# Performance work log

Measured on AMD Instinct MI355X. Metric: run time of the kernel, lower is better.

## Reference

```python
import jax, jax.numpy as jnp
import numpy as np

H, A, V = 8, 32, 32
NODE_IN, EDGE_IN, NODE_OUT, EDGE_OUT = 128, 64, 128, 64


def setup_inputs() -> dict:
    key = jax.random.key(0)
    ks = jax.random.split(key, 8)
    B, N = 1, 384
    s = lambda fan: 1.0 / np.sqrt(fan).astype(np.float32)
    nodes = jax.random.normal(ks[0], (B, NODE_IN, N), jnp.float32)
    edges = jax.random.normal(ks[1], (B, EDGE_IN, N, N), jnp.float32)
    mask = jax.random.randint(ks[2], (B, N), 0, 2).astype(bool)
    W_q = jax.random.normal(ks[3], (A * H, NODE_IN), jnp.float32) * s(NODE_IN)
    W_k = jax.random.normal(ks[4], (A * H, NODE_IN + EDGE_IN), jnp.float32) * s(NODE_IN + EDGE_IN)
    W_v = jax.random.normal(ks[5], (V * H, NODE_IN + EDGE_IN), jnp.float32) * s(NODE_IN + EDGE_IN)
    W_o = jax.random.normal(ks[6], (NODE_OUT, V * H), jnp.float32) * s(V * H)
    W_e = jax.random.normal(ks[7], (EDGE_OUT, V * H + EDGE_IN), jnp.float32) * s(V * H + EDGE_IN)
    return dict(nodes=nodes, edges=edges, mask=mask, W_q=W_q, W_k=W_k, W_v=W_v, W_o=W_o, W_e=W_e)


def reference(nodes, edges, mask, W_q, W_k, W_v, W_o, W_e):
    B, C, N = nodes.shape
    # 1x1 convs are channel matmuls
    query = jnp.einsum('oc,bcn->bon', W_q, nodes)                      # [B, H*A, N]
    node_edges = jnp.concatenate(
        [jnp.broadcast_to(nodes[:, :, :, None], (B, C, N, N)), edges], axis=1)  # [B, C+E, N, N]
    key = jnp.einsum('oc,bcij->boij', W_k, node_edges)                 # [B, H*A, N, N]
    value = jnp.einsum('oc,bcij->boij', W_v, node_edges).reshape(B, H, V, N, N)
    # elementwise QK: query broadcast over column axis j
    sim = (query[:, :, :, None] * key).reshape(B, H, A, N, N).sum(axis=2)
    sim = sim / jnp.sqrt(jnp.asarray(A, sim.dtype))                    # [B, H, N, N]
    sim = jnp.where(mask[:, None, None, :], sim, -jnp.inf)
    sim = jax.nn.softmax(sim, axis=-1)
    mm = (mask[:, None, :, None] & mask[:, None, None, :]).astype(sim.dtype)  # [B,1,N,N]
    sim = sim * mm
    value = value * mm[:, None]
    node_features = jnp.einsum('bhij,bhvij->bhvi', sim, value).reshape(B, H * V, N)
    node_out = jnp.einsum('od,bdn->bon', W_o, node_features)           # [B, node_out, N]
    # symmetrized edge features: (f_i + f_j) / 2, then concat raw edges
    ef = (node_features[:, :, :, None] + node_features[:, :, None, :]) * 0.5  # [B,H*V,N,N]
    ef = jnp.concatenate([ef, edges], axis=1)
    edge_out = jnp.einsum('oc,bcij->boij', W_e, ef)                    # [B, edge_out, N, N]
    return node_out, edge_out
```

## Files before the change

### kernel.cpp

```cpp
#include <hip/hip_runtime.h>
#include <math.h>

#define NN 384
#define NSQ (NN*NN)

#define WS_MASKF 0
#define WS_C1    384
#define WS_P     3456
#define WS_VN    200064
#define WS_T     298368
#define WS_GH    494976
#define WS_WT    519552
#define WS_WOT   523648
#define WS_WVE   556416
#define WS_WEN   572800

typedef short short8 __attribute__((ext_vector_type(8)));
typedef float f32x4 __attribute__((ext_vector_type(4)));

__device__ __forceinline__ unsigned short f2bf(float x) {
    unsigned u = __float_as_uint(x);
    return (unsigned short)((u + 0x7FFFu + ((u >> 16) & 1u)) >> 16);
}

__global__ __launch_bounds__(256) void k_proj(
    const float* __restrict__ nodes, const float* __restrict__ Wq,
    const float* __restrict__ Wk, const float* __restrict__ Wv,
    const float* __restrict__ Wo, const float* __restrict__ We,
    const unsigned int* __restrict__ mi, float* __restrict__ ws) {
    int tid = threadIdx.x;
    if (blockIdx.x >= 96) {
        if (blockIdx.x == 96) {
            __shared__ int bytemode;
            if (tid == 0) bytemode = 0;
            __syncthreads();
            unsigned v0 = mi[tid];
            unsigned v1 = (tid < 128) ? mi[256 + tid] : 0u;
            if (v0 > 1u || v1 > 1u) bytemode = 1;
            __syncthreads();
            float* maskf = ws + WS_MASKF;
            for (int j = tid; j < NN; j += 256) {
                int on;
                if (bytemode) on = (((const unsigned char*)mi)[j] != 0);
                else          on = (mi[j] != 0u);
                maskf[j] = on ? 1.0f : 0.0f;
            }
        } else if (blockIdx.x == 97) {
            unsigned short* WtBF = reinterpret_cast<unsigned short*>(ws + WS_WT);
            for (int idx = tid; idx < 4096; idx += 256) {
                int o = idx >> 6, c = idx & 63;
                WtBF[o * 64 + c] = f2bf(We[o * 320 + 256 + c]);
            }
        } else if (blockIdx.x == 98) {
            float* WoT = ws + WS_WOT;
            for (int idx = tid; idx < 32768; idx += 256) {
                int dd = idx >> 7, o = idx & 127;
                WoT[dd * 128 + o] = Wo[o * 256 + dd];
            }
        } else if (blockIdx.x == 99) {
            float* WvE = ws + WS_WVE;
            for (int idx = tid; idx < 16384; idx += 256) {
                int c = idx >> 8, d = idx & 255;
                WvE[c * 256 + d] = Wv[d * 192 + 128 + c];
            }
        } else {
            float* WeN = ws + WS_WEN;
            for (int idx = tid; idx < 16384; idx += 256) {
                int dd = idx >> 6, o = idx & 63;
                WeN[dd * 64 + o] = We[o * 320 + dd];
            }
        }
        return;
    }
    float* c1_ws = ws + WS_C1;
    float* P_ws  = ws + WS_P;
    float* vn_ws = ws + WS_VN;
    int i0 = blockIdx.x * 4;
    __shared__ float nl[128][4];
    __shared__ float q_l[256][4];
    __shared__ float qk_l[256][4];
    for (int idx = tid; idx < 512; idx += 256) {
        int m = idx >> 2, ii = idx & 3;
        nl[m][ii] = nodes[m * NN + i0 + ii];
    }
    __syncthreads();
    int o = tid;
    float aq[4], ak[4], av[4];
#pragma unroll
    for (int ii = 0; ii < 4; ii++) { aq[ii] = 0.f; ak[ii] = 0.f; av[ii] = 0.f; }
    {
        const float4* wq4 = reinterpret_cast<const float4*>(Wq + o * 128);
        const float4* wk4 = reinterpret_cast<const float4*>(Wk + o * 192);
        const float4* wv4 = reinterpret_cast<const float4*>(Wv + o * 192);
#pragma unroll 8
        for (int m4 = 0; m4 < 32; m4++) {
            float4 wq = wq4[m4];
            float4 wk = wk4[m4];
            float4 wv = wv4[m4];
#pragma unroll
            for (int s = 0; s < 4; s++) {
                int m = m4 * 4 + s;
                float fq = s == 0 ? wq.x : s == 1 ? wq.y : s == 2 ? wq.z : wq.w;
                float fk = s == 0 ? wk.x : s == 1 ? wk.y : s == 2 ? wk.z : wk.w;
                float fv = s == 0 ? wv.x : s == 1 ? wv.y : s == 2 ? wv.z : wv.w;
#pragma unroll
                for (int ii = 0; ii < 4; ii++) {
                    float nv = nl[m][ii];
                    aq[ii] = fmaf(fq, nv, aq[ii]);
                    ak[ii] = fmaf(fk, nv, ak[ii]);
                    av[ii] = fmaf(fv, nv, av[ii]);
                }
            }
        }
    }
#pragma unroll
    for (int ii = 0; ii < 4; ii++) {
        vn_ws[(size_t)(i0 + ii) * 256 + o] = av[ii];
        q_l[o][ii]  = aq[ii];
        qk_l[o][ii] = aq[ii] * ak[ii];
    }
    __syncthreads();
    if (tid < 32) {
        int h = tid >> 2, ii = tid & 3;
        float s = 0.f;
        for (int a = 0; a < 32; a++) s += qk_l[h * 32 + a][ii];
        c1_ws[(i0 + ii) * 8 + h] = s;
    }
    for (int rep = 0; rep < 2; rep++) {
        int idx = rep * 256 + tid;
        int c = idx & 63, h = idx >> 6;
        float ap[4];
#pragma unroll
        for (int ii = 0; ii < 4; ii++) ap[ii] = 0.f;
        for (int a = 0; a < 32; a++) {
            float w = Wk[(h * 32 + a) * 192 + 128 + c];
#pragma unroll
            for (int ii = 0; ii < 4; ii++)
                ap[ii] = fmaf(q_l[h * 32 + a][ii], w, ap[ii]);
        }
#pragma unroll
        for (int ii = 0; ii < 4; ii++)
            P_ws[(size_t)(i0 + ii) * 512 + c * 8 + h] = ap[ii];
    }
}

__global__ __launch_bounds__(512) void k_attn(
    const float* __restrict__ edges, const float* __restrict__ ws_ro,
    float* __restrict__ gh_ws, float* __restrict__ out) {
    __shared__ __align__(16) unsigned short epad_h[64 * 392];
    __shared__ __align__(16) float sT2[NN * 8];
    __shared__ __align__(16) float T_lds[512];
    __shared__ float nf_lds[256];
    const float* maskf = ws_ro + WS_MASKF;
    const float* c1w   = ws_ro + WS_C1;
    const float* Pw    = ws_ro + WS_P;
    const float* vn_ws = ws_ro + WS_VN;
    const float* WvE   = ws_ro + WS_WVE;
    const float* WoT   = ws_ro + WS_WOT;
    const float* WeN   = ws_ro + WS_WEN;
    int i = blockIdx.x;
    int tid = threadIdx.x;
    int wv = tid >> 6, ln = tid & 63;
    float mask_i = maskf[i];

    if (tid < NN) {
        int j = tid;
        const float* eb = edges + (size_t)i * NN + j;
        const float* Pi = Pw + (size_t)i * 512;
        float acc[8];
#pragma unroll
        for (int h = 0; h < 8; h++) acc[h] = 0.f;
#pragma unroll
        for (int cb = 0; cb < 4; cb++) {
            float ev[16];
#pragma unroll
            for (int t = 0; t < 16; t++)
                ev[t] = eb[(size_t)(cb * 16 + t) * NSQ];
#pragma unroll
            for (int t = 0; t < 16; t++) {
                int c = cb * 16 + t;
                epad_h[c * 392 + j] = f2bf(ev[t]);
                const float* Pc = Pi + c * 8;
#pragma unroll
                for (int h = 0; h < 8; h++) acc[h] = fmaf(Pc[h], ev[t], acc[h]);
            }
        }
        float mj = maskf[j];
        const float* c1i = c1w + i * 8;
        float sv[8];
#pragma unroll
        for (int h = 0; h < 8; h++) {
            float s = (c1i[h] + acc[h]) * 0.17677669529663687f;
            sv[h] = (mj != 0.0f) ? s : -1e30f;
        }
        *reinterpret_cast<float4*>(&sT2[j * 8])     = make_float4(sv[0], sv[1], sv[2], sv[3]);
        *reinterpret_cast<float4*>(&sT2[j * 8 + 4]) = make_float4(sv[4], sv[5], sv[6], sv[7]);
    }
    __syncthreads();
    float v[6];
    {
        int h = wv;
#pragma unroll
        for (int k = 0; k < 6; k++) v[k] = sT2[(ln + 64 * k) * 8 + h];
    }
    __syncthreads();
    {
        int h = wv;
        float m = v[0];
#pragma unroll
        for (int k = 1; k < 6; k++) m = fmaxf(m, v[k]);
#pragma unroll
        for (int s = 1; s < 64; s <<= 1) m = fmaxf(m, __shfl_xor(m, s));
        float ex[6]; float sum = 0.f;
#pragma unroll
        for (int k = 0; k < 6; k++) { ex[k] = __expf(v[k] - m); sum += ex[k]; }
#pragma unroll
        for (int s = 1; s < 64; s <<= 1) sum += __shfl_xor(sum, s);
        float fac = mask_i / sum;
        unsigned short* s_bf = reinterpret_cast<unsigned short*>(sT2);
#pragma unroll
        for (int k = 0; k < 6; k++)
            s_bf[h * 392 + ln + 64 * k] = f2bf(ex[k] * fac);
    }
    __syncthreads();
    if (tid < 256) {
        const unsigned short* s_bf = reinterpret_cast<const unsigned short*>(sT2);
        int nc   = ln & 15;
        int quad = ln >> 4;
        int hrow = nc & 7;
        f32x4 acc = {0.f, 0.f, 0.f, 0.f};
#pragma unroll
        for (int s = 0; s < 12; s++) {
            int jb = s * 32 + quad * 8;
            short8 a = *reinterpret_cast<const short8*>(&s_bf[hrow * 392 + jb]);
            short8 b = *reinterpret_cast<const short8*>(&epad_h[(wv * 16 + nc) * 392 + jb]);
            acc = __builtin_amdgcn_mfma_f32_16x16x32_bf16(a, b, acc, 0, 0, 0);
        }
        if (ln < 32) {
#pragma unroll
            for (int r = 0; r < 4; r++) {
                int h = quad * 4 + r;
                T_lds[h * 64 + wv * 16 + nc] = acc[r];
            }
        }
    }
    __syncthreads();
    if (tid < 256) {
        int d = tid, h = d >> 5;
        float a0 = 0.f, a1 = 0.f, a2 = 0.f, a3 = 0.f;
#pragma unroll
        for (int c = 0; c < 64; c += 4) {
            a0 = fmaf(WvE[(c    ) * 256 + d], T_lds[h * 64 + c    ], a0);
            a1 = fmaf(WvE[(c + 1) * 256 + d], T_lds[h * 64 + c + 1], a1);
            a2 = fmaf(WvE[(c + 2) * 256 + d], T_lds[h * 64 + c + 2], a2);
            a3 = fmaf(WvE[(c + 3) * 256 + d], T_lds[h * 64 + c + 3], a3);
        }
        nf_lds[d] = mask_i * vn_ws[(size_t)i * 256 + d] + ((a0 + a1) + (a2 + a3));
    }
    __syncthreads();
    if (tid < 128) {
        int o = tid;
        float b0 = 0.f, b1 = 0.f, b2 = 0.f, b3 = 0.f;
#pragma unroll 8
        for (int dd = 0; dd < 256; dd += 4) {
            b0 = fmaf(WoT[(dd    ) * 128 + o], nf_lds[dd    ], b0);
            b1 = fmaf(WoT[(dd + 1) * 128 + o], nf_lds[dd + 1], b1);
            b2 = fmaf(WoT[(dd + 2) * 128 + o], nf_lds[dd + 2], b2);
            b3 = fmaf(WoT[(dd + 3) * 128 + o], nf_lds[dd + 3], b3);
        }
        out[o * NN + i] = (b0 + b1) + (b2 + b3);
    } else if (tid < 192) {
        int o = tid - 128;
        float b0 = 0.f, b1 = 0.f, b2 = 0.f, b3 = 0.f;
#pragma unroll 8
        for (int dd = 0; dd < 256; dd += 4) {
            b0 = fmaf(WeN[(dd    ) * 64 + o], nf_lds[dd    ], b0);
            b1 = fmaf(WeN[(dd + 1) * 64 + o], nf_lds[dd + 1], b1);
            b2 = fmaf(WeN[(dd + 2) * 64 + o], nf_lds[dd + 2], b2);
            b3 = fmaf(WeN[(dd + 3) * 64 + o], nf_lds[dd + 3], b3);
        }
        gh_ws[o * NN + i] = 0.5f * ((b0 + b1) + (b2 + b3));
    }
}

__global__ __launch_bounds__(192) void k_edge(
    const float* __restrict__ edges, const float* __restrict__ ws_ro,
    float* __restrict__ out_e) {
    __shared__ __align__(16) unsigned short eT[48 * 72];
    const unsigned short* WtBF = reinterpret_cast<const unsigned short*>(ws_ro + WS_WT);
    const float* gh = ws_ro + WS_GH;
    int i = blockIdx.x, jh = blockIdx.y, tid = threadIdx.x;

    {
        int ch = tid / 48, jl = tid - ch * 48;
        int c0 = ch * 16;
        const float* eb = edges + (size_t)c0 * NSQ + (size_t)i * NN + jh * 48 + jl;
        float ev[16];
#pragma unroll
        for (int t = 0; t < 16; t++)
            ev[t] = eb[(size_t)t * NSQ];
        short8 p0, p1;
#pragma unroll
        for (int t = 0; t < 8; t++) p0[t] = (short)f2bf(ev[t]);
#pragma unroll
        for (int t = 0; t < 8; t++) p1[t] = (short)f2bf(ev[t + 8]);
        *reinterpret_cast<short8*>(&eT[jl * 72 + c0])     = p0;
        *reinterpret_cast<short8*>(&eT[jl * 72 + c0 + 8]) = p1;
    }
    __syncthreads();

    int L = tid & 63, wv = tid >> 6;
    int nc = L & 15, quad = L >> 4;
    short8 a00 = *reinterpret_cast<const short8*>(&WtBF[(0 * 16 + nc) * 64 + 0  + quad * 8]);
    short8 a01 = *reinterpret_cast<const short8*>(&WtBF[(0 * 16 + nc) * 64 + 32 + quad * 8]);
    short8 a10 = *reinterpret_cast<const short8*>(&WtBF[(1 * 16 + nc) * 64 + 0  + quad * 8]);
    short8 a11 = *reinterpret_cast<const short8*>(&WtBF[(1 * 16 + nc) * 64 + 32 + quad * 8]);
    short8 a20 = *reinterpret_cast<const short8*>(&WtBF[(2 * 16 + nc) * 64 + 0  + quad * 8]);
    short8 a21 = *reinterpret_cast<const short8*>(&WtBF[(2 * 16 + nc) * 64 + 32 + quad * 8]);
    short8 a30 = *reinterpret_cast<const short8*>(&WtBF[(3 * 16 + nc) * 64 + 0  + quad * 8]);
    short8 a31 = *reinterpret_cast<const short8*>(&WtBF[(3 * 16 + nc) * 64 + 32 + quad * 8]);
    float ghi[16];
#pragma unroll
    for (int ot = 0; ot < 4; ot++)
#pragma unroll
        for (int r = 0; r < 4; r++)
            ghi[ot * 4 + r] = gh[(ot * 16 + quad * 4 + r) * NN + i];

    {
        int jt = wv;
        short8 b0 = *reinterpret_cast<const short8*>(&eT[(jt * 16 + nc) * 72 + 0  + quad * 8]);
        short8 b1 = *reinterpret_cast<const short8*>(&eT[(jt * 16 + nc) * 72 + 32 + quad * 8]);
        int j = jh * 48 + jt * 16 + nc;
        f32x4 c0 = {0.f, 0.f, 0.f, 0.f};
        f32x4 c1 = {0.f, 0.f, 0.f, 0.f};
        f32x4 c2 = {0.f, 0.f, 0.f, 0.f};
        f32x4 c3 = {0.f, 0.f, 0.f, 0.f};
        c0 = __builtin_amdgcn_mfma_f32_16x16x32_bf16(a00, b0, c0, 0, 0, 0);
        c0 = __builtin_amdgcn_mfma_f32_16x16x32_bf16(a01, b1, c0, 0, 0, 0);
        c1 = __builtin_amdgcn_mfma_f32_16x16x32_bf16(a10, b0, c1, 0, 0, 0);
        c1 = __builtin_amdgcn_mfma_f32_16x16x32_bf16(a11, b1, c1, 0, 0, 0);
        c2 = __builtin_amdgcn_mfma_f32_16x16x32_bf16(a20, b0, c2, 0, 0, 0);
        c2 = __builtin_amdgcn_mfma_f32_16x16x32_bf16(a21, b1, c2, 0, 0, 0);
        c3 = __builtin_amdgcn_mfma_f32_16x16x32_bf16(a30, b0, c3, 0, 0, 0);
        c3 = __builtin_amdgcn_mfma_f32_16x16x32_bf16(a31, b1, c3, 0, 0, 0);
#pragma unroll
        for (int ot = 0; ot < 4; ot++) {
            f32x4 cc = ot == 0 ? c0 : ot == 1 ? c1 : ot == 2 ? c2 : c3;
#pragma unroll
            for (int r = 0; r < 4; r++) {
                int o = ot * 16 + quad * 4 + r;
                float val = cc[r] + ghi[ot * 4 + r] + gh[o * NN + j];
                __builtin_nontemporal_store(val, &out_e[(size_t)o * NSQ + (size_t)i * NN + j]);
            }
        }
    }
}

extern "C" void kernel_launch(void* const* d_in, const int* in_sizes, int n_in,
                              void* d_out, int out_size, void* d_ws, size_t ws_size,
                              hipStream_t stream) {
    const float* nodes = (const float*)d_in[0];
    const float* edges = (const float*)d_in[1];
    const unsigned int* mask = (const unsigned int*)d_in[2];
    const float* Wq = (const float*)d_in[3];
    const float* Wk = (const float*)d_in[4];
    const float* Wv = (const float*)d_in[5];
    const float* Wo = (const float*)d_in[6];
    const float* We = (const float*)d_in[7];
    float* out = (float*)d_out;
    float* ws  = (float*)d_ws;
    float* out_e = out + 128 * NN;

    hipLaunchKernelGGL(k_proj, dim3(101), dim3(256), 0, stream,
                       nodes, Wq, Wk, Wv, Wo, We, mask, ws);
    hipLaunchKernelGGL(k_attn, dim3(384), dim3(512), 0, stream,
                       edges, ws, ws + WS_GH, out);
    hipLaunchKernelGGL(k_edge, dim3(384, 8), dim3(192), 0, stream,
                       edges, ws, out_e);
}
```

Before: 143.5 us.

## Split attention over column halves with flash-style softmax merge kernel

```diff
diff --git a/kernel.cpp b/kernel.cpp
--- a/kernel.cpp
+++ b/kernel.cpp
@@ -8,12 +8,13 @@
 #define WS_C1    384
 #define WS_P     3456
 #define WS_VN    200064
-#define WS_T     298368
 #define WS_GH    494976
 #define WS_WT    519552
 #define WS_WOT   523648
 #define WS_WVE   556416
 #define WS_WEN   572800
+#define WS_TP    602112
+#define WS_MS    995328
 
 typedef short short8 __attribute__((ext_vector_type(8)));
 typedef float f32x4 __attribute__((ext_vector_type(4)));
@@ -21,6 +22,9 @@
 __device__ __forceinline__ unsigned short f2bf(float x) {
     unsigned u = __float_as_uint(x);
     return (unsigned short)((u + 0x7FFFu + ((u >> 16) & 1u)) >> 16);
+}
+__device__ __forceinline__ float bf2f(unsigned short b) {
+    return __uint_as_float(((unsigned)b) << 16);
 }
 
 __global__ __launch_bounds__(256) void k_proj(
@@ -145,45 +149,54 @@
 }
 
 __global__ __launch_bounds__(512) void k_attn(
-    const float* __restrict__ edges, const float* __restrict__ ws_ro,
-    float* __restrict__ gh_ws, float* __restrict__ out) {
-    __shared__ __align__(16) unsigned short epad_h[64 * 392];
-    __shared__ __align__(16) float sT2[NN * 8];
-    __shared__ __align__(16) float T_lds[512];
-    __shared__ float nf_lds[256];
-    const float* maskf = ws_ro + WS_MASKF;
-    const float* c1w   = ws_ro + WS_C1;
-    const float* Pw    = ws_ro + WS_P;
-    const float* vn_ws = ws_ro + WS_VN;
-    const float* WvE   = ws_ro + WS_WVE;
-    const float* WoT   = ws_ro + WS_WOT;
-    const float* WeN   = ws_ro + WS_WEN;
-    int i = blockIdx.x;
+    const float* __restrict__ edges, float* __restrict__ ws) {
+    __shared__ __align__(16) unsigned short epad_h[64 * 200];
+    __shared__ __align__(16) float sT2[192 * 8];
+    const float* maskf = ws + WS_MASKF;
+    const float* c1w   = ws + WS_C1;
+    const float* Pw    = ws + WS_P;
+    int i = blockIdx.x, jh = blockIdx.y;
     int tid = threadIdx.x;
     int wv = tid >> 6, ln = tid & 63;
-    float mask_i = maskf[i];
-
-    if (tid < NN) {
-        int j = tid;
-        const float* eb = edges + (size_t)i * NN + j;
+
+    {
+        int c = tid >> 3, g = tid & 7;
+        const float* src = edges + (size_t)c * NSQ + (size_t)i * NN + jh * 192 + g * 24;
+        float4 v0 = reinterpret_cast<const float4*>(src)[0];
+        float4 v1 = reinterpret_cast<const float4*>(src)[1];
+        float4 v2 = reinterpret_cast<const float4*>(src)[2];
+        float4 v3 = reinterpret_cast<const float4*>(src)[3];
+        float4 v4 = reinterpret_cast<const float4*>(src)[4];
+        float4 v5 = reinterpret_cast<const float4*>(src)[5];
+        unsigned short* dst = &epad_h[c * 200 + g * 24];
+#define PACK2(A, B, OFS)                                                     \
+        {                                                                    \
+            short8 p;                                                        \
+            p[0] = (short)f2bf(A.x); p[1] = (short)f2bf(A.y);                \
+            p[2] = (short)f2bf(A.z); p[3] = (short)f2bf(A.w);                \
+            p[4] = (short)f2bf(B.x); p[5] = (short)f2bf(B.y);                \
+            p[6] = (short)f2bf(B.z); p[7] = (short)f2bf(B.w);                \
+            *reinterpret_cast<short8*>(dst + (OFS)) = p;                     \
+        }
+        PACK2(v0, v1, 0)
+        PACK2(v2, v3, 8)
+        PACK2(v4, v5, 16)
+#undef PACK2
+    }
+    __syncthreads();
+
+    if (tid < 192) {
+        int j_loc = tid, j = jh * 192 + j_loc;
         const float* Pi = Pw + (size_t)i * 512;
         float acc[8];
 #pragma unroll
         for (int h = 0; h < 8; h++) acc[h] = 0.f;
-#pragma unroll
-        for (int cb = 0; cb < 4; cb++) {
-            float ev[16];
-#pragma unroll
-            for (int t = 0; t < 16; t++)
-                ev[t] = eb[(size_t)(cb * 16 + t) * NSQ];
-#pragma unroll
-            for (int t = 0; t < 16; t++) {
-                int c = cb * 16 + t;
-                epad_h[c * 392 + j] = f2bf(ev[t]);
-                const float* Pc = Pi + c * 8;
-#pragma unroll
-                for (int h = 0; h < 8; h++) acc[h] = fmaf(Pc[h], ev[t], acc[h]);
-            }
+#pragma unroll 8
+        for (int c = 0; c < 64; c++) {
+            float ev = bf2f(epad_h[c * 200 + j_loc]);
+            const float* Pc = Pi + c * 8;
+#pragma unroll
+            for (int h = 0; h < 8; h++) acc[h] = fmaf(Pc[h], ev, acc[h]);
         }
         float mj = maskf[j];
         const float* c1i = c1w + i * 8;
@@ -193,34 +206,35 @@
             float s = (c1i[h] + acc[h]) * 0.17677669529663687f;
             sv[h] = (mj != 0.0f) ? s : -1e30f;
         }
-        *reinterpret_cast<float4*>(&sT2[j * 8])     = make_float4(sv[0], sv[1], sv[2], sv[3]);
-        *reinterpret_cast<float4*>(&sT2[j * 8 + 4]) = make_float4(sv[4], sv[5], sv[6], sv[7]);
-    }
-    __syncthreads();
-    float v[6];
+        *reinterpret_cast<float4*>(&sT2[j_loc * 8])     = make_float4(sv[0], sv[1], sv[2], sv[3]);
+        *reinterpret_cast<float4*>(&sT2[j_loc * 8 + 4]) = make_float4(sv[4], sv[5], sv[6], sv[7]);
+    }
+    __syncthreads();
+    float v[3];
     {
         int h = wv;
 #pragma unroll
-        for (int k = 0; k < 6; k++) v[k] = sT2[(ln + 64 * k) * 8 + h];
+        for (int k = 0; k < 3; k++) v[k] = sT2[(ln + 64 * k) * 8 + h];
     }
     __syncthreads();
     {
         int h = wv;
-        float m = v[0];
-#pragma unroll
-        for (int k = 1; k < 6; k++) m = fmaxf(m, v[k]);
+        float m = fmaxf(fmaxf(v[0], v[1]), v[2]);
 #pragma unroll
         for (int s = 1; s < 64; s <<= 1) m = fmaxf(m, __shfl_xor(m, s));
-        float ex[6]; float sum = 0.f;
-#pragma unroll
-        for (int k = 0; k < 6; k++) { ex[k] = __expf(v[k] - m); sum += ex[k]; }
+        float ex[3]; float sum = 0.f;
+#pragma unroll
+        for (int k = 0; k < 3; k++) { ex[k] = __expf(v[k] - m); sum += ex[k]; }
 #pragma unroll
         for (int s = 1; s < 64; s <<= 1) sum += __shfl_xor(sum, s);
-        float fac = mask_i / sum;
         unsigned short* s_bf = reinterpret_cast<unsigned short*>(sT2);
 #pragma unroll
-        for (int k = 0; k < 6; k++)
-            s_bf[h * 392 + ln + 64 * k] = f2bf(ex[k] * fac);
+        for (int k = 0; k < 3; k++)
+            s_bf[h * 200 + ln + 64 * k] = f2bf(ex[k]);
+        if (ln == 0) {
+            ws[WS_MS + (i * 2 + jh) * 8 + h] = m;
+            ws[WS_MS + 6144 + (i * 2 + jh) * 8 + h] = sum;
+        }
     }
     __syncthreads();
     if (tid < 256) {
@@ -230,32 +244,71 @@
         int hrow = nc & 7;
         f32x4 acc = {0.f, 0.f, 0.f, 0.f};
 #pragma unroll
-        for (int s = 0; s < 12; s++) {
+        for (int s = 0; s < 6; s++) {
             int jb = s * 32 + quad * 8;
-            short8 a = *reinterpret_cast<const short8*>(&s_bf[hrow * 392 + jb]);
-            short8 b = *reinterpret_cast<const short8*>(&epad_h[(wv * 16 + nc) * 392 + jb]);
+            short8 a = *reinterpret_cast<const short8*>(&s_bf[hrow * 200 + jb]);
+            short8 b = *reinterpret_cast<const short8*>(&epad_h[(wv * 16 + nc) * 200 + jb]);
             acc = __builtin_amdgcn_mfma_f32_16x16x32_bf16(a, b, acc, 0, 0, 0);
         }
         if (ln < 32) {
+            float* Tp = ws + WS_TP + (size_t)(i * 2 + jh) * 512;
 #pragma unroll
             for (int r = 0; r < 4; r++) {
                 int h = quad * 4 + r;
-                T_lds[h * 64 + wv * 16 + nc] = acc[r];
-            }
-        }
-    }
-    __syncthreads();
-    if (tid < 256) {
+                Tp[h * 64 + wv * 16 + nc] = acc[r];
+            }
+        }
+    }
+}
+
+__global__ __launch_bounds__(256) void k_comb(
+    const float* __restrict__ ws_ro, float* __restrict__ gh_ws,
+    float* __restrict__ out) {
+    __shared__ __align__(16) float T_l[512];
+    __shared__ float nf_l[256];
+    __shared__ float a1s[8], a2s[8];
+    const float* maskf = ws_ro + WS_MASKF;
+    const float* vn_ws = ws_ro + WS_VN;
+    const float* WvE   = ws_ro + WS_WVE;
+    const float* WoT   = ws_ro + WS_WOT;
+    const float* WeN   = ws_ro + WS_WEN;
+    int i = blockIdx.x, tid = threadIdx.x;
+    float mask_i = maskf[i];
+    if (tid < 8) {
+        int h = tid;
+        float m1 = ws_ro[WS_MS + (i * 2 + 0) * 8 + h];
+        float m2 = ws_ro[WS_MS + (i * 2 + 1) * 8 + h];
+        float s1 = ws_ro[WS_MS + 6144 + (i * 2 + 0) * 8 + h];
+        float s2 = ws_ro[WS_MS + 6144 + (i * 2 + 1) * 8 + h];
+        float m = fmaxf(m1, m2);
+        float w1 = __expf(m1 - m), w2 = __expf(m2 - m);
+        float fac = mask_i / (w1 * s1 + w2 * s2);
+        a1s[h] = w1 * fac;
+        a2s[h] = w2 * fac;
+    }
+    __syncthreads();
+    {
+        const float* T1 = ws_ro + WS_TP + (size_t)(i * 2 + 0) * 512;
+        const float* T2 = ws_ro + WS_TP + (size_t)(i * 2 + 1) * 512;
+#pragma unroll
+        for (int r = 0; r < 2; r++) {
+            int t = tid + r * 256;
+            int h = t >> 6;
+            T_l[t] = a1s[h] * T1[t] + a2s[h] * T2[t];
+        }
+    }
+    __syncthreads();
+    {
         int d = tid, h = d >> 5;
         float a0 = 0.f, a1 = 0.f, a2 = 0.f, a3 = 0.f;
 #pragma unroll
         for (int c = 0; c < 64; c += 4) {
-            a0 = fmaf(WvE[(c    ) * 256 + d], T_lds[h * 64 + c    ], a0);
-            a1 = fmaf(WvE[(c + 1) * 256 + d], T_lds[h * 64 + c + 1], a1);
-            a2 = fmaf(WvE[(c + 2) * 256 + d], T_lds[h * 64 + c + 2], a2);
-            a3 = fmaf(WvE[(c + 3) * 256 + d], T_lds[h * 64 + c + 3], a3);
-        }
-        nf_lds[d] = mask_i * vn_ws[(size_t)i * 256 + d] + ((a0 + a1) + (a2 + a3));
+            a0 = fmaf(WvE[(c    ) * 256 + d], T_l[h * 64 + c    ], a0);
+            a1 = fmaf(WvE[(c + 1) * 256 + d], T_l[h * 64 + c + 1], a1);
+            a2 = fmaf(WvE[(c + 2) * 256 + d], T_l[h * 64 + c + 2], a2);
+            a3 = fmaf(WvE[(c + 3) * 256 + d], T_l[h * 64 + c + 3], a3);
+        }
+        nf_l[d] = mask_i * vn_ws[(size_t)i * 256 + d] + ((a0 + a1) + (a2 + a3));
     }
     __syncthreads();
     if (tid < 128) {
@@ -263,10 +316,10 @@
         float b0 = 0.f, b1 = 0.f, b2 = 0.f, b3 = 0.f;
 #pragma unroll 8
         for (int dd = 0; dd < 256; dd += 4) {
-            b0 = fmaf(WoT[(dd    ) * 128 + o], nf_lds[dd    ], b0);
-            b1 = fmaf(WoT[(dd + 1) * 128 + o], nf_lds[dd + 1], b1);
-            b2 = fmaf(WoT[(dd + 2) * 128 + o], nf_lds[dd + 2], b2);
-            b3 = fmaf(WoT[(dd + 3) * 128 + o], nf_lds[dd + 3], b3);
+            b0 = fmaf(WoT[(dd    ) * 128 + o], nf_l[dd    ], b0);
+            b1 = fmaf(WoT[(dd + 1) * 128 + o], nf_l[dd + 1], b1);
+            b2 = fmaf(WoT[(dd + 2) * 128 + o], nf_l[dd + 2], b2);
+            b3 = fmaf(WoT[(dd + 3) * 128 + o], nf_l[dd + 3], b3);
         }
         out[o * NN + i] = (b0 + b1) + (b2 + b3);
     } else if (tid < 192) {
@@ -274,10 +327,10 @@
         float b0 = 0.f, b1 = 0.f, b2 = 0.f, b3 = 0.f;
 #pragma unroll 8
         for (int dd = 0; dd < 256; dd += 4) {
-            b0 = fmaf(WeN[(dd    ) * 64 + o], nf_lds[dd    ], b0);
-            b1 = fmaf(WeN[(dd + 1) * 64 + o], nf_lds[dd + 1], b1);
-            b2 = fmaf(WeN[(dd + 2) * 64 + o], nf_lds[dd + 2], b2);
-            b3 = fmaf(WeN[(dd + 3) * 64 + o], nf_lds[dd + 3], b3);
+            b0 = fmaf(WeN[(dd    ) * 64 + o], nf_l[dd    ], b0);
+            b1 = fmaf(WeN[(dd + 1) * 64 + o], nf_l[dd + 1], b1);
+            b2 = fmaf(WeN[(dd + 2) * 64 + o], nf_l[dd + 2], b2);
+            b3 = fmaf(WeN[(dd + 3) * 64 + o], nf_l[dd + 3], b3);
         }
         gh_ws[o * NN + i] = 0.5f * ((b0 + b1) + (b2 + b3));
     }
@@ -373,8 +426,10 @@
 
     hipLaunchKernelGGL(k_proj, dim3(101), dim3(256), 0, stream,
                        nodes, Wq, Wk, Wv, Wo, We, mask, ws);
-    hipLaunchKernelGGL(k_attn, dim3(384), dim3(512), 0, stream,
-                       edges, ws, ws + WS_GH, out);
+    hipLaunchKernelGGL(k_attn, dim3(384, 2), dim3(512), 0, stream,
+                       edges, ws);
+    hipLaunchKernelGGL(k_comb, dim3(384), dim3(256), 0, stream,
+                       ws, ws + WS_GH, out);
     hipLaunchKernelGGL(k_edge, dim3(384, 8), dim3(192), 0, stream,
                        edges, ws, out_e);
 }
```

Result: no change. 145.4 us (+1.3%).
